# Kernel tuning notes

Hardware: AMD Instinct MI355X
Metric: run time of the kernel (lower is better)

The kernel has to match this reference:

```python
import jax, jax.numpy as jnp
import numpy as np

B, M, N, D, C = 4, 256, 64, 512, 1024  # batch, frames, tokens, d_model, n_classes


def setup_inputs() -> dict:
    key = jax.random.key(0)
    ks = jax.random.split(key, 6)
    s = 1.0 / np.sqrt(D)
    return {
        "encoder_out": jax.random.normal(ks[0], (B, M, D), jnp.float32),
        "decoder_out": jax.random.normal(ks[1], (B, N, D), jnp.float32),
        "W1": jax.random.normal(ks[2], (D, 2 * D), jnp.float32) * s,  # torch Linear [out,in], in=joint_size=2*d_model
        "b1": jax.random.normal(ks[3], (D,), jnp.float32) * s,
        "W2": jax.random.normal(ks[4], (C, D), jnp.float32) * s,
        "b2": jax.random.normal(ks[5], (C,), jnp.float32) * s,
    }


def reference(encoder_out, decoder_out, W1, b1, W2, b2):
    # cat([enc, dec], -1) @ W1.T == enc @ W1[:, :D].T + dec @ W1[:, D:].T
    # so project each side separately, then broadcast-add (avoids the [B,M,N,2D] concat).
    d = encoder_out.shape[-1]
    proj_enc = jnp.einsum("bmd,kd->bmk", encoder_out, W1[:, :d])   # [B,M,D]
    proj_dec = jnp.einsum("bnd,kd->bnk", decoder_out, W1[:, d:])   # [B,N,D]
    hidden = jnp.tanh(proj_enc[:, :, None, :] + proj_dec[:, None, :, :] + b1)  # [B,M,N,D]
    logits = jnp.einsum("bmnd,cd->bmnc", hidden, W2) + b2          # [B,M,N,C]
    return jax.nn.log_softmax(logits, axis=-1)
```

## Files before the change

### kernel.cpp

```cpp
#include <hip/hip_runtime.h>
#include <hip/hip_bf16.h>
#include <stdint.h>


typedef __bf16         bf16x8 __attribute__((ext_vector_type(8)));
typedef float          f32x4  __attribute__((ext_vector_type(4)));
typedef float          f32x16 __attribute__((ext_vector_type(16)));
typedef unsigned short u16x8  __attribute__((ext_vector_type(8)));

__device__ __forceinline__ unsigned short f2bf(float f) {
  unsigned int u = __float_as_uint(f);
  u += 0x7fffu + ((u >> 16) & 1u);
  return (unsigned short)(u >> 16);
}

__device__ __forceinline__ f32x4 mfma16(u16x8 a, u16x8 b, f32x4 c) {
  return __builtin_amdgcn_mfma_f32_16x16x32_bf16(
      __builtin_bit_cast(bf16x8, a), __builtin_bit_cast(bf16x8, b), c, 0, 0, 0);
}
__device__ __forceinline__ f32x16 mfma32(u16x8 a, u16x8 b, f32x16 c) {
  return __builtin_amdgcn_mfma_f32_32x32x16_bf16(
      __builtin_bit_cast(bf16x8, a), __builtin_bit_cast(bf16x8, b), c, 0, 0, 0);
}

__global__ __launch_bounds__(256) void prep_kernel(
    const float* __restrict__ enc, const float* __restrict__ dec,
    const float* __restrict__ W1,  const float* __restrict__ W2,
    unsigned short* __restrict__ encB, unsigned short* __restrict__ decB,
    unsigned short* __restrict__ W1eB, unsigned short* __restrict__ W1dB,
    unsigned short* __restrict__ W2t)
{
  const int i = blockIdx.x * 256 + threadIdx.x;
  encB[i] = f2bf(enc[i]);
  {
    const int e  = i & 7;
    const int l  = (i >> 3) & 63;
    const int cb = (i >> 9) & 1;
    const int ks = (i >> 10) & 31;
    const int w  = i >> 15;
    const int col = w * 64 + cb * 32 + (l & 31);
    const int k   = ks * 16 + (l >> 5) * 8 + e;
    W2t[i] = f2bf(W2[col * 512 + k]);
  }
  if (i < 262144) {
    const int k = i >> 9, d = i & 511;
    W1eB[i] = f2bf(W1[k * 1024 + d]);
    W1dB[i] = f2bf(W1[k * 1024 + 512 + d]);
  }
  if (i < 131072) decB[i] = f2bf(dec[i]);
}

__global__ __launch_bounds__(256) void proj_kernel(
    const unsigned short* __restrict__ A, const unsigned short* __restrict__ Wt,
    const float* __restrict__ bias, float* __restrict__ out)
{
  const int rtile = blockIdx.x >> 3;
  const int ctile = blockIdx.x & 7;
  const int w = threadIdx.x >> 6;
  const int l = threadIdx.x & 63;
  const int q = l >> 4, ln = l & 15;

  f32x4 acc[4] = {};
  const unsigned short* Ab = A  + (size_t)(rtile * 64 + ln) * 512 + q * 8;
  const unsigned short* Wb = Wt + (size_t)(ctile * 64 + w * 16 + ln) * 512 + q * 8;

#pragma unroll 4
  for (int ks = 0; ks < 16; ++ks) {
    u16x8 bv = *(const u16x8*)(Wb + ks * 32);
#pragma unroll
    for (int rf = 0; rf < 4; ++rf) {
      u16x8 av = *(const u16x8*)(Ab + rf * 16 * 512 + ks * 32);
      acc[rf] = mfma16(av, bv, acc[rf]);
    }
  }
  const int col = ctile * 64 + w * 16 + ln;
  const float bv = bias ? bias[col] : 0.0f;
#pragma unroll
  for (int rf = 0; rf < 4; ++rf)
#pragma unroll
    for (int j = 0; j < 4; ++j)
      out[(size_t)(rtile * 64 + rf * 16 + q * 4 + j) * 512 + col] = acc[rf][j] + bv;
}

__global__ __launch_bounds__(1024) void joint_kernel(
    const float* __restrict__ pe, const float* __restrict__ pd,
    const unsigned short* __restrict__ W2t, const float* __restrict__ b2,
    float* __restrict__ out)
{
  __shared__ unsigned short A_sh[64 * 512];
  __shared__ float red[64][17];
  __shared__ float lse_sh[64];

  const int blk = blockIdx.x;
  const int b   = blk >> 8;
  const int tid = threadIdx.x;
  const int w = tid >> 6, l = tid & 63;
  const int lo = l & 31, hi = l >> 5;

  {
    const float* per = pe + (size_t)blk * 512 + l * 8;
    const float4 pe0 = *(const float4*)(per);
    const float4 pe1 = *(const float4*)(per + 4);
#pragma unroll
    for (int r = 0; r < 4; ++r) {
      const int n = (w << 2) | r;
      const float* pdr = pd + (size_t)((b << 6) | n) * 512 + l * 8;
      const float4 q0 = *(const float4*)(pdr);
      const float4 q1 = *(const float4*)(pdr + 4);
      float x[8] = {pe0.x + q0.x, pe0.y + q0.y, pe0.z + q0.z, pe0.w + q0.w,
                    pe1.x + q1.x, pe1.y + q1.y, pe1.z + q1.z, pe1.w + q1.w};
      u16x8 pk;
#pragma unroll
      for (int e = 0; e < 8; ++e) {
        const float ex = __expf(2.0f * x[e]);
        const float tv = 1.0f - 2.0f * __builtin_amdgcn_rcpf(ex + 1.0f);
        pk[e] = f2bf(tv);
      }
      *(u16x8*)((char*)A_sh + n * 1024 + ((l ^ (n & 7)) << 4)) = pk;
    }
  }
  __syncthreads();

  f32x16 acc[2][2];
#pragma unroll
  for (int rb = 0; rb < 2; ++rb)
#pragma unroll
    for (int cb = 0; cb < 2; ++cb) acc[rb][cb] = (f32x16)(0.f);

  const char* Abase = (const char*)A_sh + lo * 1024;
  const int x7 = lo & 7;
  const unsigned short* Wb = W2t + (size_t)w * 32768 + l * 8;

  for (int ks = 0; ks < 32; ++ks) {
    u16x8 bv[2], av[2];
#pragma unroll
    for (int cb = 0; cb < 2; ++cb)
      bv[cb] = *(const u16x8*)(Wb + ks * 1024 + cb * 512);
#pragma unroll
    for (int rb = 0; rb < 2; ++rb)
      av[rb] = *(const u16x8*)(Abase + rb * 32768 + (((2 * ks + hi) ^ x7) << 4));
#pragma unroll
    for (int rb = 0; rb < 2; ++rb)
#pragma unroll
      for (int cb = 0; cb < 2; ++cb)
        acc[rb][cb] = mfma32(av[rb], bv[cb], acc[rb][cb]);
  }

  const float L2E = 1.4426950408889634f;
  const float LN2 = 0.6931471805599453f;
  float b2v[2];
#pragma unroll
  for (int cb = 0; cb < 2; ++cb) b2v[cb] = b2[w * 64 + cb * 32 + lo];

#pragma unroll
  for (int rb = 0; rb < 2; ++rb) {
    float s[16];
#pragma unroll
    for (int reg = 0; reg < 16; ++reg) {
      const float x0 = acc[rb][0][reg] + b2v[0];
      const float x1 = acc[rb][1][reg] + b2v[1];
      acc[rb][0][reg] = x0;
      acc[rb][1][reg] = x1;
      s[reg] = __builtin_amdgcn_exp2f(x0 * L2E) + __builtin_amdgcn_exp2f(x1 * L2E);
    }
#pragma unroll
    for (int o = 1; o < 32; o <<= 1)
#pragma unroll
      for (int reg = 0; reg < 16; ++reg)
        s[reg] += __shfl_xor(s[reg], o);
    if (lo == 0) {
#pragma unroll
      for (int reg = 0; reg < 16; ++reg) {
        const int row = rb * 32 + (reg & 3) + 8 * (reg >> 2) + 4 * hi;
        red[row][w] = s[reg];
      }
    }
  }
  __syncthreads();

  if (tid < 64) {
    float s = red[tid][0];
#pragma unroll
    for (int ww = 1; ww < 16; ++ww) s += red[tid][ww];
    lse_sh[tid] = LN2 * __builtin_amdgcn_logf(s);
  }
  __syncthreads();

  float* outb = out + (size_t)blk * 65536 + w * 64 + lo;
#pragma unroll
  for (int rb = 0; rb < 2; ++rb)
#pragma unroll
    for (int reg = 0; reg < 16; ++reg) {
      const int row = rb * 32 + (reg & 3) + 8 * (reg >> 2) + 4 * hi;
      const float lse = lse_sh[row];
      float* orow = outb + (size_t)row * 1024;
      orow[0]  = acc[rb][0][reg] - lse;
      orow[32] = acc[rb][1][reg] - lse;
    }
}

extern "C" void kernel_launch(void* const* d_in, const int* in_sizes, int n_in,
                              void* d_out, int out_size, void* d_ws, size_t ws_size,
                              hipStream_t stream) {
  (void)in_sizes; (void)n_in; (void)out_size; (void)ws_size;
  const float* enc = (const float*)d_in[0];
  const float* dec = (const float*)d_in[1];
  const float* W1  = (const float*)d_in[2];
  const float* b1  = (const float*)d_in[3];
  const float* W2  = (const float*)d_in[4];
  const float* b2  = (const float*)d_in[5];
  float* out = (float*)d_out;

  char* ws = (char*)d_ws;
  unsigned short* encB = (unsigned short*)(ws + 0);
  unsigned short* decB = (unsigned short*)(ws + 1048576);
  unsigned short* W1eB = (unsigned short*)(ws + 1310720);
  unsigned short* W1dB = (unsigned short*)(ws + 1835008);
  unsigned short* W2t  = (unsigned short*)(ws + 2359296);
  float*          pe   = (float*)(ws + 3407872);
  float*          pd   = (float*)(ws + 5505024);

  prep_kernel<<<2048, 256, 0, stream>>>(enc, dec, W1, W2, encB, decB, W1eB, W1dB, W2t);
  proj_kernel<<<128, 256, 0, stream>>>(encB, W1eB, nullptr, pe);
  proj_kernel<<< 32, 256, 0, stream>>>(decB, W1dB, b1,      pd);
  joint_kernel<<<1024, 1024, 0, stream>>>(pe, pd, W2t, b2, out);
}
```

Baseline: 157.5 us.

## Double-buffer W2 tiles into LDS via async global_load_lds and merge projection launches

The joint kernel now streams each wave's W2 slice into a per-wave double-buffered LDS region using global-to-LDS direct loads. The load for the next k-step is issued while the current one is consumed, with explicit vmcnt waits and scheduling barriers, so global latency is hidden behind the MFMAs. The bias load is moved before the tanh stage so it overlaps too. The two projection launches are fused into one 160-block launch to save a kernel launch. The extra 64KB of LDS per block raises shared-memory use to about 133KB, which may limit occupancy, and the hand-written waitcnt must stay correct.

```diff
diff --git a/kernel.cpp b/kernel.cpp
--- a/kernel.cpp
+++ b/kernel.cpp
@@ -21,6 +21,12 @@
 __device__ __forceinline__ f32x16 mfma32(u16x8 a, u16x8 b, f32x16 c) {
   return __builtin_amdgcn_mfma_f32_32x32x16_bf16(
       __builtin_bit_cast(bf16x8, a), __builtin_bit_cast(bf16x8, b), c, 0, 0, 0);
+}
+
+__device__ __forceinline__ void stage16(const void* g, void* l) {
+  __builtin_amdgcn_global_load_lds(
+      (const __attribute__((address_space(1))) void*)g,
+      (__attribute__((address_space(3))) void*)l, 16, 0, 0);
 }
 
 __global__ __launch_bounds__(256) void prep_kernel(
@@ -51,11 +57,18 @@
 }
 
 __global__ __launch_bounds__(256) void proj_kernel(
-    const unsigned short* __restrict__ A, const unsigned short* __restrict__ Wt,
-    const float* __restrict__ bias, float* __restrict__ out)
+    const unsigned short* __restrict__ encB, const unsigned short* __restrict__ decB,
+    const unsigned short* __restrict__ W1eB, const unsigned short* __restrict__ W1dB,
+    const float* __restrict__ b1, float* __restrict__ pe, float* __restrict__ pd)
 {
-  const int rtile = blockIdx.x >> 3;
-  const int ctile = blockIdx.x & 7;
+  int bid = blockIdx.x;
+  const unsigned short *A, *Wt;
+  const float* bias;
+  float* out;
+  if (bid < 128) { A = encB; Wt = W1eB; bias = nullptr; out = pe; }
+  else           { bid -= 128; A = decB; Wt = W1dB; bias = b1; out = pd; }
+  const int rtile = bid >> 3;
+  const int ctile = bid & 7;
   const int w = threadIdx.x >> 6;
   const int l = threadIdx.x & 63;
   const int q = l >> 4, ln = l & 15;
@@ -88,6 +101,7 @@
     float* __restrict__ out)
 {
   __shared__ unsigned short A_sh[64 * 512];
+  __shared__ unsigned short B_sh[16 * 2048];
   __shared__ float red[64][17];
   __shared__ float lse_sh[64];
 
@@ -96,6 +110,17 @@
   const int tid = threadIdx.x;
   const int w = tid >> 6, l = tid & 63;
   const int lo = l & 31, hi = l >> 5;
+
+  const unsigned short* Wsrc = W2t + (size_t)w * 32768;
+  unsigned short* Bdst = B_sh + w * 2048;
+
+  stage16(Wsrc + l * 8,       Bdst);
+  stage16(Wsrc + 512 + l * 8, Bdst + 512);
+
+  float b2v[2];
+#pragma unroll
+  for (int cb = 0; cb < 2; ++cb) b2v[cb] = b2[w * 64 + cb * 32 + lo];
+  asm volatile("" :: "v"(b2v[0]), "v"(b2v[1]));
 
   {
     const float* per = pe + (size_t)blk * 512 + l * 8;
@@ -129,13 +154,25 @@
 
   const char* Abase = (const char*)A_sh + lo * 1024;
   const int x7 = lo & 7;
-  const unsigned short* Wb = W2t + (size_t)w * 32768 + l * 8;
-
+  const unsigned short* Bread = B_sh + w * 2048 + l * 8;
+
+#pragma unroll
   for (int ks = 0; ks < 32; ++ks) {
+    __builtin_amdgcn_sched_barrier(0);
+    if (ks < 31) {
+      stage16(Wsrc + (ks + 1) * 1024 + l * 8,       Bdst + ((ks + 1) & 1) * 1024);
+      stage16(Wsrc + (ks + 1) * 1024 + 512 + l * 8, Bdst + ((ks + 1) & 1) * 1024 + 512);
+      __builtin_amdgcn_sched_barrier(0);
+      asm volatile("s_waitcnt vmcnt(2)" ::: "memory");
+    } else {
+      asm volatile("s_waitcnt vmcnt(0)" ::: "memory");
+    }
+    __builtin_amdgcn_sched_barrier(0);
+
     u16x8 bv[2], av[2];
 #pragma unroll
     for (int cb = 0; cb < 2; ++cb)
-      bv[cb] = *(const u16x8*)(Wb + ks * 1024 + cb * 512);
+      bv[cb] = *(const u16x8*)(Bread + (ks & 1) * 1024 + cb * 512);
 #pragma unroll
     for (int rb = 0; rb < 2; ++rb)
       av[rb] = *(const u16x8*)(Abase + rb * 32768 + (((2 * ks + hi) ^ x7) << 4));
@@ -148,9 +185,6 @@
 
   const float L2E = 1.4426950408889634f;
   const float LN2 = 0.6931471805599453f;
-  float b2v[2];
-#pragma unroll
-  for (int cb = 0; cb < 2; ++cb) b2v[cb] = b2[w * 64 + cb * 32 + lo];
 
 #pragma unroll
   for (int rb = 0; rb < 2; ++rb) {
@@ -221,7 +255,6 @@
   float*          pd   = (float*)(ws + 5505024);
 
   prep_kernel<<<2048, 256, 0, stream>>>(enc, dec, W1, W2, encB, decB, W1eB, W1dB, W2t);
-  proj_kernel<<<128, 256, 0, stream>>>(encB, W1eB, nullptr, pe);
-  proj_kernel<<< 32, 256, 0, stream>>>(decB, W1dB, b1,      pd);
+  proj_kernel<<<160, 256, 0, stream>>>(encB, decB, W1eB, W1dB, b1, pe, pd);
   joint_kernel<<<1024, 1024, 0, stream>>>(pe, pd, W2t, b2, out);
 }
```

Result: faster. 152.0 us (-3.5%).
